# Optimization experiments

Hardware: AMD Instinct MI355X
Metric: run time of the kernel (lower is better)

Reference implementation:

```python
import jax, jax.numpy as jnp
import numpy as np

N = 64        # number of diagonal SSM eigenvalues
L = 262144    # l_max == sequence length


def setup_inputs() -> dict:
    key = jax.random.key(0)
    k1, k2, k3 = jax.random.split(key, 3)
    u = jax.random.normal(k1, (L,), dtype=jnp.float32)
    # scaling='linear' initializers from the module
    A_re = -0.5 * jnp.ones((N,), dtype=jnp.float32)
    A_im = jnp.pi * jnp.arange(N, dtype=jnp.float32)
    C = (0.5 ** 0.5) * jax.random.normal(k2, (N, 2), dtype=jnp.float32)
    D = jnp.ones((1,), dtype=jnp.float32)
    # log_step_initializer: uniform in [log(1e-3), log(1e-1)]
    lo, hi = np.log(1e-3), np.log(1e-1)
    log_step = jax.random.uniform(k3, (1,), dtype=jnp.float32) * (hi - lo) + lo
    return {"u": u, "A_re": A_re, "A_im": A_im, "C": C, "D": D, "log_step": log_step}


def reference(u, A_re, A_im, C, D, log_step):
    Lseq = u.shape[0]
    step = jnp.exp(log_step)                      # (1,)
    A = (A_re + 1j * A_im).astype(jnp.complex64)  # (N,) diagonal eigenvalues
    Ct = (C[:, 0] + 1j * C[:, 1]).astype(jnp.complex64)  # (N,)
    dtA = step.astype(jnp.complex64) * A          # (N,)
    # s4d_kernel_zoh: K[l] = Re[ sum_n C_n * (exp(dt*A_n)-1)/A_n * exp(l*dt*A_n) ]
    coeff = Ct * (jnp.exp(dtA) - 1.0) / A         # (N,)
    t = jnp.arange(Lseq)                          # (L,)
    vand = jnp.exp(dtA[:, None] * t)              # (N, L) Vandermonde, complex64
    K = jnp.real(coeff[:, None] * vand).sum(0).astype(u.dtype)  # (L,)
    # causal_convolution via FFT: pad both to 2L, multiply spectra, truncate
    ud = jnp.fft.rfft(jnp.pad(u, (0, Lseq)))
    Kd = jnp.fft.rfft(jnp.pad(K, (0, Lseq)))
    y = jnp.fft.irfft(ud * Kd)[:Lseq]
    return y + D * u
```

## Files before the change

### kernel.cpp

```cpp
#include <hip/hip_runtime.h>
#include <math.h>

#define L_SEQ  262144
#define NEIG   64
#define CHUNKS 2048
#define BLEN   128
#define SPAN   (CHUNKS / 64)

__global__ __launch_bounds__(64) void s4d_carry_kernel(
    const float* __restrict__ u,
    const float* __restrict__ A_re,
    const float* __restrict__ A_im,
    const float* __restrict__ log_step,
    float2* __restrict__ carries)
{
    __shared__ float u_lds[BLEN];
    const int c    = blockIdx.x;
    const int lane = threadIdx.x;

    ((float2*)u_lds)[lane] = ((const float2*)(u + c * BLEN))[lane];
    __syncthreads();

    const double dt = exp((double)log_step[0]);
    const double ar = (double)A_re[lane], ai = (double)A_im[lane];
    const double m  = exp(dt * ar);
    const float zr = (float)(m * cos(dt * ai));
    const float zi = (float)(m * sin(dt * ai));

    float xr = 0.f, xi = 0.f;
    #pragma unroll 8
    for (int t = 0; t < BLEN; ++t) {
        const float uv = u_lds[t];
        const float nr = fmaf(zr, xr, fmaf(-zi, xi, uv));
        const float ni = fmaf(zi, xr, zr * xi);
        xr = nr; xi = ni;
    }
    carries[c * NEIG + lane] = make_float2(xr, xi);
}

__global__ __launch_bounds__(64) void s4d_scan_kernel(
    const float* __restrict__ A_re,
    const float* __restrict__ A_im,
    const float* __restrict__ log_step,
    float2* __restrict__ carries)
{
    __shared__ float2 bspan[64];
    __shared__ float2 excl[64];
    const int n    = blockIdx.x;
    const int lane = threadIdx.x;

    const double dt = exp((double)log_step[0]);
    const double ar = (double)A_re[n], ai = (double)A_im[n];
    const double mB = exp(dt * ar * BLEN);
    const double aB = dt * ai * (double)BLEN;
    const float zBr = (float)(mB * cos(aB));
    const float zBi = (float)(mB * sin(aB));

    float br = 0.f, bi = 0.f;
    const int c0 = lane * SPAN;
    for (int k = 0; k < SPAN; ++k) {
        const float2 s = carries[(c0 + k) * NEIG + n];
        const float nr = fmaf(zBr, br, fmaf(-zBi, bi, s.x));
        const float ni = fmaf(zBi, br, fmaf(zBr, bi, s.y));
        br = nr; bi = ni;
    }
    bspan[lane] = make_float2(br, bi);
    __syncthreads();

    if (lane == 0) {
        const double mW = exp(dt * ar * (double)BLEN * SPAN);
        const double aW = dt * ai * (double)BLEN * SPAN;
        const float Wr = (float)(mW * cos(aW));
        const float Wi = (float)(mW * sin(aW));
        float Xr = 0.f, Xi = 0.f;
        for (int l = 0; l < 64; ++l) {
            excl[l] = make_float2(Xr, Xi);
            const float2 b = bspan[l];
            const float nr = fmaf(Wr, Xr, fmaf(-Wi, Xi, b.x));
            const float ni = fmaf(Wi, Xr, fmaf(Wr, Xi, b.y));
            Xr = nr; Xi = ni;
        }
    }
    __syncthreads();

    float2 X = excl[lane];
    float xr = X.x, xi = X.y;
    for (int k = 0; k < SPAN; ++k) {
        const int idx = (c0 + k) * NEIG + n;
        const float2 s = carries[idx];
        carries[idx] = make_float2(xr, xi);
        const float nr = fmaf(zBr, xr, fmaf(-zBi, xi, s.x));
        const float ni = fmaf(zBi, xr, fmaf(zBr, xi, s.y));
        xr = nr; xi = ni;
    }
}

__global__ __launch_bounds__(64) void s4d_out_kernel(
    const float* __restrict__ u,
    const float* __restrict__ A_re,
    const float* __restrict__ A_im,
    const float* __restrict__ Cmat,
    const float* __restrict__ Dv,
    const float* __restrict__ log_step,
    const float2* __restrict__ prefix,
    float* __restrict__ y)
{
    __shared__ float u_lds[BLEN];
    const int c    = blockIdx.x;
    const int lane = threadIdx.x;

    ((float2*)u_lds)[lane] = ((const float2*)(u + c * BLEN))[lane];
    __syncthreads();

    const double dt = exp((double)log_step[0]);
    const double ar = (double)A_re[lane], ai = (double)A_im[lane];
    const double m  = exp(dt * ar);
    const double zr_d = m * cos(dt * ai);
    const double zi_d = m * sin(dt * ai);
    const double er = zr_d - 1.0, ei = zi_d;
    const double den = ar * ar + ai * ai;
    const double qr = (er * ar + ei * ai) / den;
    const double qi = (ei * ar - er * ai) / den;
    const double cr = (double)Cmat[2 * lane], ci = (double)Cmat[2 * lane + 1];
    const float gr = (float)(cr * qr - ci * qi);
    const float gi = (float)(cr * qi + ci * qr);
    const float zr = (float)zr_d, zi = (float)zi_d;
    const float Dval = Dv[0];

    const float2 X = prefix[c * NEIG + lane];
    float xr = X.x, xi = X.y;
    float* yc = y + c * BLEN;

    #pragma unroll
    for (int q = 0; q < BLEN / 64; ++q) {
        float yk = 0.f;
        for (int j = 0; j < 64; ++j) {
            const float uv = u_lds[q * 64 + j];
            const float nr = fmaf(zr, xr, fmaf(-zi, xi, uv));
            const float ni = fmaf(zi, xr, zr * xi);
            xr = nr; xi = ni;
            float r = fmaf(gr, xr, -gi * xi);
            r += __shfl_xor(r, 1, 64);
            r += __shfl_xor(r, 2, 64);
            r += __shfl_xor(r, 4, 64);
            r += __shfl_xor(r, 8, 64);
            r += __shfl_xor(r, 16, 64);
            r += __shfl_xor(r, 32, 64);
            if (lane == j) yk = fmaf(Dval, uv, r);
        }
        yc[q * 64 + lane] = yk;
    }
}

extern "C" void kernel_launch(void* const* d_in, const int* in_sizes, int n_in,
                              void* d_out, int out_size, void* d_ws, size_t ws_size,
                              hipStream_t stream)
{
    const float* u    = (const float*)d_in[0];
    const float* A_re = (const float*)d_in[1];
    const float* A_im = (const float*)d_in[2];
    const float* Cmat = (const float*)d_in[3];
    const float* Dv   = (const float*)d_in[4];
    const float* ls   = (const float*)d_in[5];
    float* y = (float*)d_out;
    float2* carr = (float2*)d_ws;

    hipLaunchKernelGGL(s4d_carry_kernel, dim3(CHUNKS), dim3(64), 0, stream,
                       u, A_re, A_im, ls, carr);
    hipLaunchKernelGGL(s4d_scan_kernel, dim3(NEIG), dim3(64), 0, stream,
                       A_re, A_im, ls, carr);
    hipLaunchKernelGGL(s4d_out_kernel, dim3(CHUNKS), dim3(64), 0, stream,
                       u, A_re, A_im, Cmat, Dv, ls, carr, y);
}
```

Baseline: 97.22 us.

## Replace per-step shuffle reductions with LDS transpose reduction and fast-math setup

The output kernel now stores each eigenvalue's per-step contribution into a padded LDS tile and reduces 32 timesteps at once across lanes. This replaces six cross-lane shuffles per timestep. Setup math also moves from double-precision exp/sin/cos to range-reduced fast float intrinsics, and the carry and scan loops are unrolled with float4 LDS reads. The fast intrinsics may lower the accuracy of the eigenvalue powers.

```diff
diff --git a/kernel.cpp b/kernel.cpp
--- a/kernel.cpp
+++ b/kernel.cpp
@@ -6,6 +6,19 @@
 #define CHUNKS 2048
 #define BLEN   128
 #define SPAN   (CHUNKS / 64)
+
+__device__ __forceinline__ float2 cexpf_rr(double mag_arg, double ang)
+{
+    const double TWO_PI  = 6.283185307179586476;
+    const double INV_2PI = 0.15915494309189533577;
+    double q    = ang * INV_2PI;
+    double frac = q - trunc(q);
+    float  af   = (float)(frac * TWO_PI);
+    float s, c;
+    __sincosf(af, &s, &c);
+    float m = __expf((float)mag_arg);
+    return make_float2(m * c, m * s);
+}
 
 __global__ __launch_bounds__(64) void s4d_carry_kernel(
     const float* __restrict__ u,
@@ -19,21 +32,25 @@
     const int lane = threadIdx.x;
 
     ((float2*)u_lds)[lane] = ((const float2*)(u + c * BLEN))[lane];
-    __syncthreads();
-
-    const double dt = exp((double)log_step[0]);
+
+    const double dt = (double)__expf(log_step[0]);
     const double ar = (double)A_re[lane], ai = (double)A_im[lane];
-    const double m  = exp(dt * ar);
-    const float zr = (float)(m * cos(dt * ai));
-    const float zi = (float)(m * sin(dt * ai));
+    const float2 z  = cexpf_rr(dt * ar, dt * ai);
+    const float zr = z.x, zi = z.y;
+    __syncthreads();
 
     float xr = 0.f, xi = 0.f;
-    #pragma unroll 8
-    for (int t = 0; t < BLEN; ++t) {
-        const float uv = u_lds[t];
-        const float nr = fmaf(zr, xr, fmaf(-zi, xi, uv));
-        const float ni = fmaf(zi, xr, zr * xi);
-        xr = nr; xi = ni;
+    #pragma unroll
+    for (int t4 = 0; t4 < BLEN / 4; ++t4) {
+        const float4 uv4 = ((const float4*)u_lds)[t4];
+        #pragma unroll
+        for (int j = 0; j < 4; ++j) {
+            const float uv = (j == 0) ? uv4.x : (j == 1) ? uv4.y
+                           : (j == 2) ? uv4.z : uv4.w;
+            const float nr = fmaf(zr, xr, fmaf(-zi, xi, uv));
+            const float ni = fmaf(zi, xr, zr * xi);
+            xr = nr; xi = ni;
+        }
     }
     carries[c * NEIG + lane] = make_float2(xr, xi);
 }
@@ -49,15 +66,14 @@
     const int n    = blockIdx.x;
     const int lane = threadIdx.x;
 
-    const double dt = exp((double)log_step[0]);
+    const double dt = (double)__expf(log_step[0]);
     const double ar = (double)A_re[n], ai = (double)A_im[n];
-    const double mB = exp(dt * ar * BLEN);
-    const double aB = dt * ai * (double)BLEN;
-    const float zBr = (float)(mB * cos(aB));
-    const float zBi = (float)(mB * sin(aB));
+    const float2 zB = cexpf_rr(dt * ar * (double)BLEN, dt * ai * (double)BLEN);
+    const float zBr = zB.x, zBi = zB.y;
 
     float br = 0.f, bi = 0.f;
     const int c0 = lane * SPAN;
+    #pragma unroll 4
     for (int k = 0; k < SPAN; ++k) {
         const float2 s = carries[(c0 + k) * NEIG + n];
         const float nr = fmaf(zBr, br, fmaf(-zBi, bi, s.x));
@@ -68,16 +84,14 @@
     __syncthreads();
 
     if (lane == 0) {
-        const double mW = exp(dt * ar * (double)BLEN * SPAN);
-        const double aW = dt * ai * (double)BLEN * SPAN;
-        const float Wr = (float)(mW * cos(aW));
-        const float Wi = (float)(mW * sin(aW));
+        const float2 W = cexpf_rr(dt * ar * (double)(BLEN * SPAN),
+                                  dt * ai * (double)(BLEN * SPAN));
         float Xr = 0.f, Xi = 0.f;
         for (int l = 0; l < 64; ++l) {
             excl[l] = make_float2(Xr, Xi);
             const float2 b = bspan[l];
-            const float nr = fmaf(Wr, Xr, fmaf(-Wi, Xi, b.x));
-            const float ni = fmaf(Wi, Xr, fmaf(Wr, Xi, b.y));
+            const float nr = fmaf(W.x, Xr, fmaf(-W.y, Xi, b.x));
+            const float ni = fmaf(W.y, Xr, fmaf(W.x, Xi, b.y));
             Xr = nr; Xi = ni;
         }
     }
@@ -85,6 +99,7 @@
 
     float2 X = excl[lane];
     float xr = X.x, xi = X.y;
+    #pragma unroll 4
     for (int k = 0; k < SPAN; ++k) {
         const int idx = (c0 + k) * NEIG + n;
         const float2 s = carries[idx];
@@ -106,49 +121,60 @@
     float* __restrict__ y)
 {
     __shared__ float u_lds[BLEN];
+    __shared__ float contrib[32 * 65];
     const int c    = blockIdx.x;
     const int lane = threadIdx.x;
 
     ((float2*)u_lds)[lane] = ((const float2*)(u + c * BLEN))[lane];
-    __syncthreads();
-
-    const double dt = exp((double)log_step[0]);
+
+    const double dt = (double)__expf(log_step[0]);
     const double ar = (double)A_re[lane], ai = (double)A_im[lane];
-    const double m  = exp(dt * ar);
-    const double zr_d = m * cos(dt * ai);
-    const double zi_d = m * sin(dt * ai);
-    const double er = zr_d - 1.0, ei = zi_d;
-    const double den = ar * ar + ai * ai;
-    const double qr = (er * ar + ei * ai) / den;
-    const double qi = (ei * ar - er * ai) / den;
-    const double cr = (double)Cmat[2 * lane], ci = (double)Cmat[2 * lane + 1];
-    const float gr = (float)(cr * qr - ci * qi);
-    const float gi = (float)(cr * qi + ci * qr);
-    const float zr = (float)zr_d, zi = (float)zi_d;
+    const float2 z  = cexpf_rr(dt * ar, dt * ai);
+    const float zr = z.x, zi = z.y;
+
+    const float arf = (float)ar, aif = (float)ai;
+    const float er = z.x - 1.f, ei = z.y;
+    const float den = arf * arf + aif * aif;
+    const float qr = (er * arf + ei * aif) / den;
+    const float qi = (ei * arf - er * aif) / den;
+    const float cr = Cmat[2 * lane], ci = Cmat[2 * lane + 1];
+    const float gr = fmaf(cr, qr, -ci * qi);
+    const float gi = fmaf(cr, qi,  ci * qr);
     const float Dval = Dv[0];
 
     const float2 X = prefix[c * NEIG + lane];
     float xr = X.x, xi = X.y;
     float* yc = y + c * BLEN;
+    const int  t_red = lane & 31;
+    const int  hoff  = (lane >> 5) << 5;
+    __syncthreads();
 
     #pragma unroll
-    for (int q = 0; q < BLEN / 64; ++q) {
-        float yk = 0.f;
-        for (int j = 0; j < 64; ++j) {
-            const float uv = u_lds[q * 64 + j];
-            const float nr = fmaf(zr, xr, fmaf(-zi, xi, uv));
-            const float ni = fmaf(zi, xr, zr * xi);
-            xr = nr; xi = ni;
-            float r = fmaf(gr, xr, -gi * xi);
-            r += __shfl_xor(r, 1, 64);
-            r += __shfl_xor(r, 2, 64);
-            r += __shfl_xor(r, 4, 64);
-            r += __shfl_xor(r, 8, 64);
-            r += __shfl_xor(r, 16, 64);
-            r += __shfl_xor(r, 32, 64);
-            if (lane == j) yk = fmaf(Dval, uv, r);
-        }
-        yc[q * 64 + lane] = yk;
+    for (int sub = 0; sub < BLEN / 32; ++sub) {
+        #pragma unroll
+        for (int t4 = 0; t4 < 8; ++t4) {
+            const float4 uv4 = ((const float4*)u_lds)[sub * 8 + t4];
+            #pragma unroll
+            for (int j = 0; j < 4; ++j) {
+                const float uv = (j == 0) ? uv4.x : (j == 1) ? uv4.y
+                               : (j == 2) ? uv4.z : uv4.w;
+                const float nr = fmaf(zr, xr, fmaf(-zi, xi, uv));
+                const float ni = fmaf(zi, xr, zr * xi);
+                xr = nr; xi = ni;
+                contrib[(t4 * 4 + j) * 65 + lane] = fmaf(gr, xr, -gi * xi);
+            }
+        }
+        __syncthreads();
+        float r = 0.f;
+        #pragma unroll
+        for (int k = 0; k < 32; ++k)
+            r += contrib[t_red * 65 + hoff + k];
+        r += __shfl_xor(r, 32, 64);
+        if (lane < 32) {
+            const float uv = u_lds[sub * 32 + lane];
+            yc[sub * 32 + lane] = fmaf(Dval, uv, r);
+        }
+        __syncthreads();
     }
 }
 
```

Measured after the change: 82.04 us. -15.6%, faster.
